# Kernel optimization log

Hardware: AMD Instinct MI355X
Metric: run time of the kernel (lower is better)

Reference implementation:

```python
import jax, jax.numpy as jnp
import numpy as np

HEADS = 48
HEAD_DIM = 64
DIM = 3072
RANK = 128
TEXT_LEN = 226
VID_LEN = 1822
B = 1
LORA_W = 1.0
EPS = 1e-5


def setup_inputs() -> dict:
    key = jax.random.key(0)
    ks = jax.random.split(key, 24)
    s = 0.02  # weight init scale
    inp = {
        "hidden_states": jax.random.normal(ks[0], (B, VID_LEN, DIM), jnp.float32),
        "encoder_hidden_states": jax.random.normal(ks[1], (B, TEXT_LEN, DIM), jnp.float32),
        "rope_cos": jax.random.uniform(ks[2], (VID_LEN, HEAD_DIM), jnp.float32),
        "rope_sin": jax.random.uniform(ks[3], (VID_LEN, HEAD_DIM), jnp.float32),
        "Wq": jax.random.normal(ks[4], (DIM, DIM), jnp.float32) * s,
        "bq": jax.random.normal(ks[5], (DIM,), jnp.float32) * s,
        "Wk": jax.random.normal(ks[6], (DIM, DIM), jnp.float32) * s,
        "bk": jax.random.normal(ks[7], (DIM,), jnp.float32) * s,
        "Wv": jax.random.normal(ks[8], (DIM, DIM), jnp.float32) * s,
        "bv": jax.random.normal(ks[9], (DIM,), jnp.float32) * s,
        "Wo": jax.random.normal(ks[10], (DIM, DIM), jnp.float32) * s,
        "bo": jax.random.normal(ks[11], (DIM,), jnp.float32) * s,
        "lq_down": jax.random.normal(ks[12], (RANK, DIM), jnp.float32) / RANK,
        "lq_up": jax.random.normal(ks[13], (DIM, RANK), jnp.float32) * s,
        "lk_down": jax.random.normal(ks[14], (RANK, DIM), jnp.float32) / RANK,
        "lk_up": jax.random.normal(ks[15], (DIM, RANK), jnp.float32) * s,
        "lv_down": jax.random.normal(ks[16], (RANK, DIM), jnp.float32) / RANK,
        "lv_up": jax.random.normal(ks[17], (DIM, RANK), jnp.float32) * s,
        "lp_down": jax.random.normal(ks[18], (RANK, DIM), jnp.float32) / RANK,
        "lp_up": jax.random.normal(ks[19], (DIM, RANK), jnp.float32) * s,
        "gamma_q": jnp.ones((HEAD_DIM,), jnp.float32),
        "beta_q": jnp.zeros((HEAD_DIM,), jnp.float32),
        "gamma_k": jnp.ones((HEAD_DIM,), jnp.float32),
        "beta_k": jnp.zeros((HEAD_DIM,), jnp.float32),
    }
    return inp


def _lora(x, down, up):
    # x: [B,S,DIM]; down: [RANK,DIM]; up: [DIM,RANK]
    return (x @ down.T) @ up.T


def _layernorm(x, gamma, beta):
    mu = jnp.mean(x, axis=-1, keepdims=True)
    var = jnp.mean(jnp.square(x - mu), axis=-1, keepdims=True)
    return (x - mu) * jax.lax.rsqrt(var + EPS) * gamma + beta


def _apply_rope(x, cos, sin):
    # diffusers apply_rotary_emb, use_real=True, unbind_dim=-1
    # x: [B,H,S,D]; cos/sin: [S,D]
    xr = x.reshape(*x.shape[:-1], HEAD_DIM // 2, 2)
    x1, x2 = xr[..., 0], xr[..., 1]
    x_rot = jnp.stack([-x2, x1], axis=-1).reshape(x.shape)
    return x * cos + x_rot * sin


def reference(hidden_states, encoder_hidden_states, rope_cos, rope_sin,
              Wq, bq, Wk, bk, Wv, bv, Wo, bo,
              lq_down, lq_up, lk_down, lk_up, lv_down, lv_up, lp_down, lp_up,
              gamma_q, beta_q, gamma_k, beta_k):
    h = jnp.concatenate([encoder_hidden_states, hidden_states], axis=1)  # [B,S,DIM]
    S = h.shape[1]

    q = h @ Wq.T + bq + _lora(h, lq_down, lq_up) * LORA_W
    k = h @ Wk.T + bk + _lora(h, lk_down, lk_up) * LORA_W
    v = h @ Wv.T + bv + _lora(h, lv_down, lv_up) * LORA_W

    def split_heads(x):  # [B,S,DIM] -> [B,H,S,D]
        return x.reshape(B, S, HEADS, HEAD_DIM).transpose(0, 2, 1, 3)

    q, k, v = split_heads(q), split_heads(k), split_heads(v)
    q = _layernorm(q, gamma_q, beta_q)
    k = _layernorm(k, gamma_k, beta_k)

    # RoPE on video tokens only
    q = q.at[:, :, TEXT_LEN:].set(_apply_rope(q[:, :, TEXT_LEN:], rope_cos, rope_sin))
    k = k.at[:, :, TEXT_LEN:].set(_apply_rope(k[:, :, TEXT_LEN:], rope_cos, rope_sin))

    # scaled dot-product attention (no mask, no dropout)
    scale = 1.0 / np.sqrt(HEAD_DIM).astype(np.float32)
    scores = jnp.einsum("bhqd,bhkd->bhqk", q, k) * scale
    probs = jax.nn.softmax(scores, axis=-1)
    attn_out = jnp.einsum("bhqk,bhkd->bhqd", probs, v)

    out = attn_out.transpose(0, 2, 1, 3).reshape(B, S, DIM)
    out = out @ Wo.T + bo + _lora(out, lp_down, lp_up) * LORA_W

    enc_out = out[:, :TEXT_LEN, :]
    hid_out = out[:, TEXT_LEN:, :]
    return (hid_out, enc_out)
```

## Files before the change

kernel.cpp:

```cpp
#include <hip/hip_runtime.h>
#include <hip/hip_bf16.h>
#include <stdint.h>

#define S_TOT 2048
#define TEXT 226
#define VID 1822
#define DIM 3072
#define NH 48
#define HD 64

typedef __bf16 bf16x8 __attribute__((ext_vector_type(8)));
typedef __bf16 bf16x4 __attribute__((ext_vector_type(4)));
typedef float f32x4 __attribute__((ext_vector_type(4)));

#define AS1 __attribute__((address_space(1)))
#define AS3 __attribute__((address_space(3)))

__device__ __forceinline__ void g2l16(const void* g, void* l) {
    __builtin_amdgcn_global_load_lds((const AS1 uint32_t*)(uintptr_t)g,
                                     (AS3 uint32_t*)(uintptr_t)l, 16, 0, 0);
}

__device__ __forceinline__ f32x4 mfma16(bf16x4 a, bf16x4 b, f32x4 c) {
#if __has_builtin(__builtin_amdgcn_mfma_f32_16x16x16bf16_1k)
    typedef short s4 __attribute__((ext_vector_type(4)));
    union U { bf16x4 b; s4 s; };
    U ua, ub; ua.b = a; ub.b = b;
    return __builtin_amdgcn_mfma_f32_16x16x16bf16_1k(ua.s, ub.s, c, 0, 0, 0);
#else
    f32x4 d = c;
    asm volatile("v_mfma_f32_16x16x16_bf16 %0, %1, %2, %0"
                 : "+v"(d) : "v"(a), "v"(b));
    return d;
#endif
}

#define ARENA_N 47431680ull

struct NormArgs { const void* p[24]; };

__global__ __launch_bounds__(256)
void normalize_inputs(NormArgs a, __bf16* __restrict__ arena)
{
    static constexpr unsigned long long segStart[25] = {
        0ull, 694272ull, 6291456ull, 15728640ull, 25165824ull, 34603008ull,
        44040192ull, 44433408ull, 44826624ull, 45219840ull, 45613056ull,
        46006272ull, 46399488ull, 46792704ull, 47185920ull, 47302528ull,
        47419136ull, 47422208ull, 47425280ull, 47428352ull, 47431424ull,
        47431488ull, 47431552ull, 47431616ull, 47431680ull };
    static constexpr int segIn[24] = {
        1, 0, 4, 6, 8, 10, 12, 13, 14, 15, 16, 17, 18, 19, 2, 3,
        5, 7, 9, 11, 20, 21, 22, 23 };

    const uint32_t w0 = *(const uint32_t*)a.p[20];
    const bool f32in = (w0 == 0x3F800000u);

    const size_t i0 = ((size_t)blockIdx.x * 256 + threadIdx.x) * 8;
    if (i0 >= ARENA_N) return;
    int s = 0;
    while (i0 >= segStart[s + 1]) s++;
    const size_t off = i0 - segStart[s];

    if (f32in) {
        const float* src = (const float*)a.p[segIn[s]] + off;
        const float4 v0 = ((const float4*)src)[0];
        const float4 v1 = ((const float4*)src)[1];
        bf16x8 o;
        o[0] = (__bf16)v0.x; o[1] = (__bf16)v0.y; o[2] = (__bf16)v0.z; o[3] = (__bf16)v0.w;
        o[4] = (__bf16)v1.x; o[5] = (__bf16)v1.y; o[6] = (__bf16)v1.z; o[7] = (__bf16)v1.w;
        *(bf16x8*)(arena + i0) = o;
    } else {
        const __bf16* src = (const __bf16*)a.p[segIn[s]] + off;
        *(uint4*)(arena + i0) = *(const uint4*)src;
    }
}

__device__ __forceinline__ void mm_chunks(
    const __bf16* __restrict__ Ag, int lda, const __bf16* __restrict__ Bg, int ldb,
    int kbeg, int kend, f32x4 (&acc)[4][4], __bf16* As, __bf16* Bs,
    int wave, int srow, int schk, int rdoff, int l15, int wm, int wn)
{
    for (int k0 = kbeg; k0 < kend; k0 += 32) {
        __syncthreads();
#pragma unroll
        for (int i = 0; i < 2; i++) {
            const int blk = i * 4 + wave;
            const int r = blk * 16 + srow;
            g2l16(Ag + (size_t)r * lda + k0 + schk, &As[blk * 512]);
            g2l16(Bg + (size_t)r * ldb + k0 + schk, &Bs[blk * 512]);
        }
        __syncthreads();
        bf16x8 af[4], bfr[4];
#pragma unroll
        for (int i = 0; i < 4; i++)
            af[i] = *(const bf16x8*)&As[(wm + i * 16 + l15) * 32 + rdoff];
#pragma unroll
        for (int j = 0; j < 4; j++)
            bfr[j] = *(const bf16x8*)&Bs[(wn + j * 16 + l15) * 32 + rdoff];
#pragma unroll
        for (int i = 0; i < 4; i++)
#pragma unroll
            for (int j = 0; j < 4; j++)
                acc[i][j] = __builtin_amdgcn_mfma_f32_16x16x32_bf16(af[i], bfr[j], acc[i][j], 0, 0, 0);
    }
}

template<int MODE>
__global__ __launch_bounds__(256)
void gemm_bt(const __bf16* __restrict__ A, int lda,
             const __bf16* __restrict__ B0, const __bf16* __restrict__ B1,
             const __bf16* __restrict__ B2, int ldb,
             const __bf16* __restrict__ bias0, const __bf16* __restrict__ bias1,
             const __bf16* __restrict__ bias2,
             __bf16* __restrict__ Cb, int ldc, int K, int tilesPerGroup,
             void* __restrict__ dout, const void* __restrict__ probe)
{
    __shared__ __bf16 As[128 * 32];
    __shared__ __bf16 Bs[128 * 32];
    const int tid  = threadIdx.x;
    const int wave = tid >> 6;
    const int lane = tid & 63;
    const int l15  = lane & 15, quad = lane >> 4;
    const int bm = blockIdx.x, bn = blockIdx.y;
    const int group = bn / tilesPerGroup;
    const int nt    = bn - group * tilesPerGroup;
    const __bf16* B    = (group == 0) ? B0 : ((group == 1) ? B1 : B2);
    const __bf16* bias = (group == 0) ? bias0 : ((group == 1) ? bias1 : bias2);

    const int srow  = lane >> 2;
    const int schk  = ((((lane & 3) - (lane >> 3)) & 3)) * 8;
    const int rdoff = ((quad + (l15 >> 1)) & 3) * 8;
    const __bf16* Ag = A + (size_t)(bm * 128) * lda;
    const __bf16* Bg = B + (size_t)(nt * 128) * ldb;

    f32x4 acc[4][4] = {};
    const int wm = (wave & 1) * 64;
    const int wn = (wave >> 1) * 64;

    mm_chunks(Ag, lda, Bg, ldb, 0, K, acc, As, Bs, wave, srow, schk, rdoff, l15, wm, wn);

    bool f32out = false;
    if (MODE == 1) f32out = (*(const uint32_t*)probe == 0x3F800000u);

#pragma unroll
    for (int i = 0; i < 4; i++) {
#pragma unroll
        for (int j = 0; j < 4; j++) {
            const int coll = wn + j * 16 + l15;
            const int col  = bn * 128 + coll;
            float bv = 0.f;
            if (bias) bv = (float)bias[nt * 128 + coll];
#pragma unroll
            for (int r = 0; r < 4; r++) {
                const int row = bm * 128 + wm + i * 16 + quad * 4 + r;
                float v = acc[i][j][r] + bv;
                if (MODE == 1) {
                    const size_t mrow = (row < TEXT) ? (size_t)(row + VID) : (size_t)(row - TEXT);
                    if (f32out) ((float*)dout)[mrow * DIM + col] = v;
                    else        ((__bf16*)dout)[mrow * DIM + col] = (__bf16)v;
                } else {
                    Cb[(size_t)row * ldc + col] = (__bf16)v;
                }
            }
        }
    }
}

#define QKV_NT 48
#define QKV_NI 24

__device__ __forceinline__ void barx() {
    asm volatile("" ::: "memory");
    __builtin_amdgcn_s_barrier();
    asm volatile("" ::: "memory");
}
__device__ __forceinline__ void vmw6() { asm volatile("s_waitcnt vmcnt(6)" ::: "memory"); }
__device__ __forceinline__ void vmw0() { asm volatile("s_waitcnt vmcnt(0)" ::: "memory"); }

__device__ __forceinline__ void stage2(const __bf16* gsrc, __bf16* lds, size_t koff) {
    g2l16(gsrc + koff,      lds);
    g2l16(gsrc + koff + 32, lds + 8192);
}

__global__ __launch_bounds__(512)
void gemm256_qkv(const __bf16* __restrict__ A,
                 const __bf16* __restrict__ B0, const __bf16* __restrict__ B1,
                 const __bf16* __restrict__ B2,
                 const __bf16* __restrict__ bias0, const __bf16* __restrict__ bias1,
                 const __bf16* __restrict__ bias2,
                 __bf16* __restrict__ C)
{
    __shared__ __bf16 L[65536];

    const int bid = blockIdx.x;
    const int swz = (bid & 7) * 32 + (bid >> 3);
    const int bm = swz & 7;
    const int bn = swz >> 3;
    const int group = bn / 12;
    const int nt    = bn - group * 12;
    const __bf16* Bm   = (group == 0) ? B0 : ((group == 1) ? B1 : B2);
    const __bf16* bias = (group == 0) ? bias0 : ((group == 1) ? bias1 : bias2);

    const int tid = threadIdx.x, wave = tid >> 6, lane = tid & 63;
    const int wr = wave >> 2, wc = wave & 3;
    const int l15 = lane & 15, quad = lane >> 4;
    const int srow  = lane >> 2;
    const int schk  = ((((lane & 3) - (lane >> 3)) & 3)) * 8;
    const int rdoff = ((quad + (l15 >> 1)) & 3) * 8;
    const int rdbase = l15 * 32 + rdoff;

    static constexpr int AL0[8] = {0,1,2,3, 8,9,10,11};
    static constexpr int AL1[8] = {4,5,6,7, 12,13,14,15};
    static constexpr int BL0[8] = {0,1,4,5, 8,9,12,13};
    static constexpr int BL1[8] = {2,3,6,7, 10,11,14,15};
    const int a0 = AL0[wave], a1 = AL1[wave], b0 = BL0[wave], b1 = BL1[wave];

    const __bf16* Ag = A  + (size_t)(bm * 256) * DIM;
    const __bf16* Bg = Bm + (size_t)(nt * 256) * DIM;
    const __bf16* gA0 = Ag + (size_t)(a0 * 16 + srow) * DIM + schk;
    const __bf16* gA1 = Ag + (size_t)(a1 * 16 + srow) * DIM + schk;
    const __bf16* gB0 = Bg + (size_t)(b0 * 16 + srow) * DIM + schk;
    const __bf16* gB1 = Bg + (size_t)(b1 * 16 + srow) * DIM + schk;

#define STG_A0(BUF, T) stage2(gA0, &L[(BUF)*32768 +         a0*512], (size_t)(T)*64)
#define STG_A1(BUF, T) stage2(gA1, &L[(BUF)*32768 +         a1*512], (size_t)(T)*64)
#define STG_B0(BUF, T) stage2(gB0, &L[(BUF)*32768 + 16384 + b0*512], (size_t)(T)*64)
#define STG_B1(BUF, T) stage2(gB1, &L[(BUF)*32768 + 16384 + b1*512], (size_t)(T)*64)

    f32x4 acc[8][4] = {};

    STG_A0(0, 0); STG_B0(0, 0); STG_A1(0, 0); STG_B1(0, 0);
    STG_A0(1, 1); STG_B0(1, 1); STG_A1(1, 1);
    vmw6();
    barx();

#define PH(BUF, MH, NH, STAGE, WAIT) do {                                        \
    bf16x8 af[4][2], bfr[2][2];                                                  \
    _Pragma("unroll")                                                            \
    for (int mm = 0; mm < 4; mm++) {                                             \
        af[mm][0] = *(const bf16x8*)&L[(BUF)*32768 +        (wr*8 + (MH)*4 + mm)*512 + rdbase]; \
        af[mm][1] = *(const bf16x8*)&L[(BUF)*32768 + 8192 + (wr*8 + (MH)*4 + mm)*512 + rdbase]; \
    }                                                                            \
    _Pragma("unroll")                                                            \
    for (int nn = 0; nn < 2; nn++) {                                             \
        bfr[nn][0] = *(const bf16x8*)&L[(BUF)*32768 + 16384 +        (wc*4 + (NH)*2 + nn)*512 + rdbase]; \
        bfr[nn][1] = *(const bf16x8*)&L[(BUF)*32768 + 16384 + 8192 + (wc*4 + (NH)*2 + nn)*512 + rdbase]; \
    }                                                                            \
    barx();                                                                      \
    STAGE;                                                                       \
    __builtin_amdgcn_s_setprio(1);                                               \
    _Pragma("unroll")                                                            \
    for (int mm = 0; mm < 4; mm++)                                               \
        _Pragma("unroll")                                                        \
        for (int nn = 0; nn < 2; nn++) {                                         \
            acc[(MH)*4+mm][(NH)*2+nn] = __builtin_amdgcn_mfma_f32_16x16x32_bf16( \
                af[mm][0], bfr[nn][0], acc[(MH)*4+mm][(NH)*2+nn], 0, 0, 0);      \
            acc[(MH)*4+mm][(NH)*2+nn] = __builtin_amdgcn_mfma_f32_16x16x32_bf16( \
                af[mm][1], bfr[nn][1], acc[(MH)*4+mm][(NH)*2+nn], 0, 0, 0);      \
        }                                                                        \
    __builtin_amdgcn_s_setprio(0);                                               \
    WAIT;                                                                        \
    barx();                                                                      \
} while (0)

#pragma unroll 1
    for (int i = 0; i < QKV_NI; i++) {
        const int t1 = 2 * i + 1, t2 = 2 * i + 2, t3 = 2 * i + 3;
        const bool more = (i < QKV_NI - 1);
        PH(0, 0, 0, { STG_B1(1, t1); },              { });
        PH(0, 0, 1, { if (more) STG_A0(0, t2); },    { });
        PH(0, 1, 0, { if (more) STG_B0(0, t2); },    { });
        PH(0, 1, 1, { if (more) STG_A1(0, t2); },    { if (more) vmw6(); else vmw0(); });
        PH(1, 0, 0, { if (more) STG_B1(0, t2); },    { });
        PH(1, 0, 1, { if (more) STG_A0(1, t3); },    { });
        PH(1, 1, 0, { if (more) STG_B0(1, t3); },    { });
        PH(1, 1, 1, { if (more) STG_A1(1, t3); },    { if (more) vmw6(); else vmw0(); });
    }
#undef PH
#undef STG_A0
#undef STG_A1
#undef STG_B0
#undef STG_B1

#pragma unroll
    for (int mh = 0; mh < 2; mh++)
#pragma unroll
    for (int nh = 0; nh < 2; nh++)
#pragma unroll
    for (int nn = 0; nn < 2; nn++) {
        const int coll = wc * 64 + nh * 32 + nn * 16 + l15;
        const float bv = (float)bias[nt * 256 + coll];
        const int col = bn * 256 + coll;
#pragma unroll
        for (int mm = 0; mm < 4; mm++) {
            const int rowb = bm * 256 + wr * 128 + mh * 64 + mm * 16 + quad * 4;
#pragma unroll
            for (int r = 0; r < 4; r++)
                C[(size_t)(rowb + r) * 9216 + col] = (__bf16)(acc[mh*4+mm][nh*2+nn][r] + bv);
        }
    }
}

struct TpArgs { const __bf16* S[4]; __bf16* D[4]; };

__global__ __launch_bounds__(256)
void transp_ld(TpArgs a)
{
    __shared__ float tile[64][65];
    const __bf16* src = a.S[blockIdx.z];
    __bf16* dst = a.D[blockIdx.z];
    const int j0 = blockIdx.x * 64;
    const int r0 = blockIdx.y * 64;
    const int tid = threadIdx.x;
    const int rr = tid >> 4;
    const int cc = (tid & 15) * 4;
#pragma unroll
    for (int p = 0; p < 4; p++) {
        const int r = p * 16 + rr;
        const uint2 raw = *(const uint2*)&src[(size_t)(r0 + r) * DIM + j0 + cc];
        const __bf16* b = (const __bf16*)&raw;
#pragma unroll
        for (int e = 0; e < 4; e++) tile[r][cc + e] = (float)b[e];
    }
    __syncthreads();
#pragma unroll
    for (int p = 0; p < 4; p++) {
        const int j = p * 16 + rr;
        __bf16 o[4];
#pragma unroll
        for (int e = 0; e < 4; e++) o[e] = (__bf16)tile[cc + e][j];
        *(uint2*)&dst[(size_t)(j0 + j) * 128 + r0 + cc] = *(const uint2*)o;
    }
}

struct FoldArgs { const __bf16* A[4]; const __bf16* B[4]; const __bf16* W[4]; __bf16* D[4]; };

__global__ __launch_bounds__(256)
void fold_w(FoldArgs a)
{
    __shared__ __bf16 As[128 * 32];
    __shared__ __bf16 Bs[128 * 32];
    const int z = blockIdx.z;
    const int tid  = threadIdx.x;
    const int wave = tid >> 6;
    const int lane = tid & 63;
    const int l15  = lane & 15, quad = lane >> 4;
    const int bm = blockIdx.x, bn = blockIdx.y;

    const int srow  = lane >> 2;
    const int schk  = ((((lane & 3) - (lane >> 3)) & 3)) * 8;
    const int rdoff = ((quad + (l15 >> 1)) & 3) * 8;
    const __bf16* Ag = a.A[z] + (size_t)(bm * 128) * 128;
    const __bf16* Bg = a.B[z] + (size_t)(bn * 128) * 128;
    const __bf16* W  = a.W[z];
    __bf16* D = a.D[z];

    f32x4 acc[4][4] = {};
    const int wm = (wave & 1) * 64;
    const int wn = (wave >> 1) * 64;

    mm_chunks(Ag, 128, Bg, 128, 0, 128, acc, As, Bs, wave, srow, schk, rdoff, l15, wm, wn);

#pragma unroll
    for (int i = 0; i < 4; i++) {
#pragma unroll
        for (int j = 0; j < 4; j++) {
            const int col = bn * 128 + wn + j * 16 + l15;
#pragma unroll
            for (int r = 0; r < 4; r++) {
                const int row = bm * 128 + wm + i * 16 + quad * 4 + r;
                const size_t idx = (size_t)row * DIM + col;
                D[idx] = (__bf16)(acc[i][j][r] + (float)W[idx]);
            }
        }
    }
}

__global__ __launch_bounds__(256)
void ln_vt(const __bf16* __restrict__ qkv,
           const __bf16* __restrict__ gq, const __bf16* __restrict__ bq,
           const __bf16* __restrict__ gk, const __bf16* __restrict__ bk,
           const __bf16* __restrict__ cosb, const __bf16* __restrict__ sinb,
           __bf16* __restrict__ qh, __bf16* __restrict__ kh,
           __bf16* __restrict__ vt)
{
    __shared__ float tile[64][65];
    if (blockIdx.x < 2048) {
        const int s = blockIdx.x;
        const int wave = threadIdx.x >> 6, lane = threadIdx.x & 63;
        for (int idx = wave; idx < 2 * NH; idx += 4) {
            const int mat  = idx / NH;
            const int head = idx - mat * NH;
            float x = (float)qkv[(size_t)s * 9216 + mat * DIM + head * HD + lane];
            float mu = x;
            mu += __shfl_xor(mu, 1, 64);  mu += __shfl_xor(mu, 2, 64);
            mu += __shfl_xor(mu, 4, 64);  mu += __shfl_xor(mu, 8, 64);
            mu += __shfl_xor(mu, 16, 64); mu += __shfl_xor(mu, 32, 64);
            mu *= 0.015625f;
            float d = x - mu;
            float vv = d * d;
            vv += __shfl_xor(vv, 1, 64);  vv += __shfl_xor(vv, 2, 64);
            vv += __shfl_xor(vv, 4, 64);  vv += __shfl_xor(vv, 8, 64);
            vv += __shfl_xor(vv, 16, 64); vv += __shfl_xor(vv, 32, 64);
            vv *= 0.015625f;
            const float g = (float)(mat ? gk[lane] : gq[lane]);
            const float b = (float)(mat ? bk[lane] : bq[lane]);
            float y = d * rsqrtf(vv + 1e-5f) * g + b;
            if (s >= TEXT) {
                const int pos = s - TEXT;
                const float c  = (float)cosb[pos * HD + lane];
                const float sn = (float)sinb[pos * HD + lane];
                const float oth = __shfl_xor(y, 1, 64);
                const float rot = (lane & 1) ? oth : -oth;
                y = y * c + rot * sn;
            }
            if (mat == 0) y *= 0.1803368801111137f;
            __bf16* dst = mat ? kh : qh;
            dst[((size_t)head * S_TOT + s) * HD + lane] = (__bf16)y;
        }
    } else {
        const int vb = blockIdx.x - 2048;
        const int h = vb >> 5, sb = vb & 31;
        const int tid = threadIdx.x;
        const int r0 = tid >> 4;
        const int c0 = (tid & 15) * 4;
#pragma unroll
        for (int p = 0; p < 4; p++) {
            const int r = p * 16 + r0;
            const uint2 raw = *(const uint2*)&qkv[((size_t)(sb * 64 + r)) * 9216 + 2 * DIM + h * HD + c0];
            const __bf16* b = (const __bf16*)&raw;
#pragma unroll
            for (int e = 0; e < 4; e++) tile[r][c0 + e] = (float)b[e];
        }
        __syncthreads();
#pragma unroll
        for (int p = 0; p < 4; p++) {
            const int d = p * 16 + r0;
            __bf16 o[4];
#pragma unroll
            for (int e = 0; e < 4; e++) o[e] = (__bf16)tile[c0 + e][d];
            *(uint2*)&vt[((size_t)(h * HD + d)) * S_TOT + sb * 64 + c0] = *(const uint2*)o;
        }
    }
}

#define KS_LD 72
#define VS_LD 146
#define NKB (S_TOT / 128)

__device__ __forceinline__ void fa_load(const __bf16* __restrict__ kh,
                                        const __bf16* __restrict__ vt,
                                        int h, int kb, int tid,
                                        bf16x8 (&kr)[4], bf16x8 (&vr)[4])
{
#pragma unroll
    for (int p = 0; p < 4; p++) {
        const int id = p * 256 + tid;
        const int krow = id >> 3, kc = (id & 7) * 8;
        kr[p] = *(const bf16x8*)(kh + ((size_t)(h * S_TOT + kb * 128 + krow)) * HD + kc);
        const int vrow = id >> 4, vc = (id & 15) * 8;
        vr[p] = *(const bf16x8*)(vt + ((size_t)(h * HD + vrow)) * S_TOT + kb * 128 + vc);
    }
}

__global__ __launch_bounds__(256)
void flash_attn(const __bf16* __restrict__ qh, const __bf16* __restrict__ kh,
                const __bf16* __restrict__ vt, __bf16* __restrict__ outp)
{
    __shared__ __bf16 Ks[128 * KS_LD];
    __shared__ __bf16 Vs[64 * VS_LD];
    const int qb = blockIdx.x, h = blockIdx.y;
    const int tid = threadIdx.x, wave = tid >> 6, lane = tid & 63;
    const int l15 = lane & 15, quad = lane >> 4;

    const __bf16* qp = qh + ((size_t)(h * S_TOT + qb * 64 + wave * 16 + l15)) * HD + quad * 8;
    const bf16x8 qf0 = *(const bf16x8*)qp;
    const bf16x8 qf1 = *(const bf16x8*)(qp + 32);

    f32x4 of[4] = {};
    float m_i = -1e30f, l_i = 0.f;

    bf16x8 kr[4], vr[4];
    fa_load(kh, vt, h, 0, tid, kr, vr);

    for (int kb = 0; kb < NKB; kb++) {
        __syncthreads();
#pragma unroll
        for (int p = 0; p < 4; p++) {
            const int id = p * 256 + tid;
            const int krow = id >> 3, kc = (id & 7) * 8;
            *(bf16x8*)&Ks[krow * KS_LD + kc] = kr[p];
            const int vrow = id >> 4, vc = (id & 15) * 8;
            *(bf16x8*)&Vs[vrow * VS_LD + vc] = vr[p];
        }
        __syncthreads();
        if (kb + 1 < NKB) fa_load(kh, vt, h, kb + 1, tid, kr, vr);

        f32x4 sf[8];
#pragma unroll
        for (int n = 0; n < 8; n++) {
            const bf16x8 k0 = *(const bf16x8*)&Ks[(n * 16 + l15) * KS_LD + quad * 8];
            const bf16x8 k1 = *(const bf16x8*)&Ks[(n * 16 + l15) * KS_LD + 32 + quad * 8];
            f32x4 z = {0.f, 0.f, 0.f, 0.f};
            z = __builtin_amdgcn_mfma_f32_16x16x32_bf16(k0, qf0, z, 0, 0, 0);
            sf[n] = __builtin_amdgcn_mfma_f32_16x16x32_bf16(k1, qf1, z, 0, 0, 0);
        }

        float mx = fmaxf(fmaxf(sf[0][0], sf[0][1]), fmaxf(sf[0][2], sf[0][3]));
#pragma unroll
        for (int n = 1; n < 8; n++)
            mx = fmaxf(mx, fmaxf(fmaxf(sf[n][0], sf[n][1]), fmaxf(sf[n][2], sf[n][3])));
        mx = fmaxf(mx, __shfl_xor(mx, 16, 64));
        mx = fmaxf(mx, __shfl_xor(mx, 32, 64));
        const float mnew = fmaxf(m_i, mx);
        const float alpha = __builtin_amdgcn_exp2f(m_i - mnew);
        m_i = mnew;
        float rs = 0.f;
#pragma unroll
        for (int n = 0; n < 8; n++)
#pragma unroll
            for (int r = 0; r < 4; r++) {
                const float pv = __builtin_amdgcn_exp2f(sf[n][r] - mnew);
                sf[n][r] = pv;
                rs += pv;
            }
        rs += __shfl_xor(rs, 16, 64);
        rs += __shfl_xor(rs, 32, 64);
        l_i = l_i * alpha + rs;

        bf16x4 pf[8];
#pragma unroll
        for (int kk = 0; kk < 8; kk++) {
            bf16x4 o;
            o[0] = (__bf16)sf[kk][0]; o[1] = (__bf16)sf[kk][1];
            o[2] = (__bf16)sf[kk][2]; o[3] = (__bf16)sf[kk][3];
            pf[kk] = o;
        }

#pragma unroll
        for (int r = 0; r < 4; r++) {
            const float a_r = __shfl(alpha, quad * 4 + r, 16);
#pragma unroll
            for (int j = 0; j < 4; j++) of[j][r] *= a_r;
        }

#pragma unroll
        for (int kk = 0; kk < 8; kk++) {
#pragma unroll
            for (int j = 0; j < 4; j++) {
                const bf16x4 vf = *(const bf16x4*)&Vs[(j * 16 + l15) * VS_LD + kk * 16 + quad * 4];
                of[j] = mfma16(pf[kk], vf, of[j]);
            }
        }
    }

#pragma unroll
    for (int r = 0; r < 4; r++) {
        const float lr = __shfl(l_i, quad * 4 + r, 16);
        const float inv = 1.f / lr;
        const int row = qb * 64 + wave * 16 + quad * 4 + r;
#pragma unroll
        for (int j = 0; j < 4; j++)
            outp[(size_t)row * DIM + h * HD + j * 16 + l15] = (__bf16)(of[j][r] * inv);
    }
}

extern "C" void kernel_launch(void* const* d_in, const int* in_sizes, int n_in,
                              void* d_out, int out_size, void* d_ws, size_t ws_size,
                              hipStream_t stream)
{
    char* ws = (char*)d_ws;
    __bf16* arena = (__bf16*)ws;

    const __bf16* h     = arena + 0;
    const __bf16* Wq    = arena + 6291456;
    const __bf16* Wk    = arena + 15728640;
    const __bf16* Wv    = arena + 25165824;
    const __bf16* Wo    = arena + 34603008;
    const __bf16* lqd   = arena + 44040192;
    const __bf16* lqu   = arena + 44433408;
    const __bf16* lkd   = arena + 44826624;
    const __bf16* lku   = arena + 45219840;
    const __bf16* lvd   = arena + 45613056;
    const __bf16* lvu   = arena + 46006272;
    const __bf16* lpd   = arena + 46399488;
    const __bf16* lpu   = arena + 46792704;
    const __bf16* ropec = arena + 47185920;
    const __bf16* ropes = arena + 47302528;
    const __bf16* bq    = arena + 47419136;
    const __bf16* bk    = arena + 47422208;
    const __bf16* bv    = arena + 47425280;
    const __bf16* bo    = arena + 47428352;
    const __bf16* gq    = arena + 47431424;
    const __bf16* btq   = arena + 47431488;
    const __bf16* gk    = arena + 47431552;
    const __bf16* btk   = arena + 47431616;

    __bf16* ldT  = (__bf16*)(ws + 94863360);
    __bf16* qkvb = (__bf16*)(ws + 98009088);
    __bf16* Wpo  = (__bf16*)(ws + 135757824);
    __bf16* Wpq  = (__bf16*)(ws + 154632192);
    __bf16* Wpk  = (__bf16*)(ws + 173506560);
    __bf16* Wpv  = (__bf16*)(ws + 192380928);
    __bf16* qh   = (__bf16*)(ws + 154632192);
    __bf16* kh   = (__bf16*)(ws + 179798016);
    __bf16* vt   = (__bf16*)(ws + 12582912);
    __bf16* attn = (__bf16*)(ws + 0);

    NormArgs na;
    for (int i = 0; i < 24; i++) na.p[i] = d_in[i];
    normalize_inputs<<<(unsigned)((ARENA_N / 8 + 255) / 256), 256, 0, stream>>>(na, arena);

    TpArgs tp;
    tp.S[0] = lqd; tp.S[1] = lkd; tp.S[2] = lvd; tp.S[3] = lpd;
    tp.D[0] = ldT; tp.D[1] = ldT + 393216; tp.D[2] = ldT + 786432; tp.D[3] = ldT + 1179648;
    transp_ld<<<dim3(48, 2, 4), 256, 0, stream>>>(tp);

    FoldArgs fa;
    fa.A[0] = lqu; fa.A[1] = lku; fa.A[2] = lvu; fa.A[3] = lpu;
    fa.B[0] = tp.D[0]; fa.B[1] = tp.D[1]; fa.B[2] = tp.D[2]; fa.B[3] = tp.D[3];
    fa.W[0] = Wq; fa.W[1] = Wk; fa.W[2] = Wv; fa.W[3] = Wo;
    fa.D[0] = Wpq; fa.D[1] = Wpk; fa.D[2] = Wpv; fa.D[3] = Wpo;
    fold_w<<<dim3(24, 24, 4), 256, 0, stream>>>(fa);

    gemm256_qkv<<<256, 512, 0, stream>>>(h, Wpq, Wpk, Wpv, bq, bk, bv, qkvb);
    gemm_bt<3><<<dim3(16, 8), 256, 0, stream>>>(
        h, DIM, Wpv + (size_t)2048 * DIM, Wpv + (size_t)2048 * DIM, Wpv + (size_t)2048 * DIM,
        DIM, bv + 2048, bv + 2048, bv + 2048,
        qkvb + 8192, 9216, DIM, 8, nullptr, nullptr);

    ln_vt<<<2048 + 1536, 256, 0, stream>>>(qkvb, gq, btq, gk, btk, ropec, ropes, qh, kh, vt);

    flash_attn<<<dim3(32, 48), 256, 0, stream>>>(qh, kh, vt, attn);

    gemm_bt<1><<<dim3(16, 24), 256, 0, stream>>>(
        attn, DIM, Wpo, Wpo, Wpo, DIM, bo, bo, bo,
        nullptr, DIM, DIM, 24, d_out, d_in[20]);
}
```

Baseline: 711.2 us.

## Shrink flash-attention KV tile to 64, raise occupancy, swizzle blocks per XCD

Halves the key/value tile per iteration from 128 to 64 rows, which cuts LDS and register use, and adds a launch-bounds occupancy hint of 6 blocks. The 2D grid becomes a 1D grid whose block index is remapped so that each XCD processes a contiguous group of heads, aiming for better L2 reuse of K/V. The trade-off is twice as many loop iterations and barriers, plus more frequent online-softmax rescaling.

```diff
diff --git a/kernel.cpp b/kernel.cpp
--- a/kernel.cpp
+++ b/kernel.cpp
@@ -444,32 +444,33 @@
     }
 }
 
-#define KS_LD 72
-#define VS_LD 146
-#define NKB (S_TOT / 128)
-
-__device__ __forceinline__ void fa_load(const __bf16* __restrict__ kh,
-                                        const __bf16* __restrict__ vt,
-                                        int h, int kb, int tid,
-                                        bf16x8 (&kr)[4], bf16x8 (&vr)[4])
-{
-#pragma unroll
-    for (int p = 0; p < 4; p++) {
+#define FA_LD 72
+#define NKB64 (S_TOT / 64)
+
+__device__ __forceinline__ void fa_load64(const __bf16* __restrict__ kh,
+                                          const __bf16* __restrict__ vt,
+                                          int h, int kb, int tid,
+                                          bf16x8 (&kr)[2], bf16x8 (&vr)[2])
+{
+#pragma unroll
+    for (int p = 0; p < 2; p++) {
         const int id = p * 256 + tid;
-        const int krow = id >> 3, kc = (id & 7) * 8;
-        kr[p] = *(const bf16x8*)(kh + ((size_t)(h * S_TOT + kb * 128 + krow)) * HD + kc);
-        const int vrow = id >> 4, vc = (id & 15) * 8;
-        vr[p] = *(const bf16x8*)(vt + ((size_t)(h * HD + vrow)) * S_TOT + kb * 128 + vc);
-    }
-}
-
-__global__ __launch_bounds__(256)
+        const int row = id >> 3;
+        const int c = (id & 7) * 8;
+        kr[p] = *(const bf16x8*)(kh + ((size_t)(h * S_TOT + kb * 64 + row)) * HD + c);
+        vr[p] = *(const bf16x8*)(vt + ((size_t)(h * HD + row)) * S_TOT + kb * 64 + c);
+    }
+}
+
+__global__ __launch_bounds__(256, 6)
 void flash_attn(const __bf16* __restrict__ qh, const __bf16* __restrict__ kh,
                 const __bf16* __restrict__ vt, __bf16* __restrict__ outp)
 {
-    __shared__ __bf16 Ks[128 * KS_LD];
-    __shared__ __bf16 Vs[64 * VS_LD];
-    const int qb = blockIdx.x, h = blockIdx.y;
+    __shared__ __bf16 Ks[64 * FA_LD];
+    __shared__ __bf16 Vs[64 * FA_LD];
+    const int swz = (blockIdx.x & 7) * 192 + (blockIdx.x >> 3);
+    const int h = swz >> 5;
+    const int qb = swz & 31;
     const int tid = threadIdx.x, wave = tid >> 6, lane = tid & 63;
     const int l15 = lane & 15, quad = lane >> 4;
 
@@ -480,27 +481,27 @@
     f32x4 of[4] = {};
     float m_i = -1e30f, l_i = 0.f;
 
-    bf16x8 kr[4], vr[4];
-    fa_load(kh, vt, h, 0, tid, kr, vr);
-
-    for (int kb = 0; kb < NKB; kb++) {
+    bf16x8 kr[2], vr[2];
+    fa_load64(kh, vt, h, 0, tid, kr, vr);
+
+    for (int kb = 0; kb < NKB64; kb++) {
         __syncthreads();
 #pragma unroll
-        for (int p = 0; p < 4; p++) {
+        for (int p = 0; p < 2; p++) {
             const int id = p * 256 + tid;
-            const int krow = id >> 3, kc = (id & 7) * 8;
-            *(bf16x8*)&Ks[krow * KS_LD + kc] = kr[p];
-            const int vrow = id >> 4, vc = (id & 15) * 8;
-            *(bf16x8*)&Vs[vrow * VS_LD + vc] = vr[p];
+            const int row = id >> 3;
+            const int c = (id & 7) * 8;
+            *(bf16x8*)&Ks[row * FA_LD + c] = kr[p];
+            *(bf16x8*)&Vs[row * FA_LD + c] = vr[p];
         }
         __syncthreads();
-        if (kb + 1 < NKB) fa_load(kh, vt, h, kb + 1, tid, kr, vr);
-
-        f32x4 sf[8];
-#pragma unroll
-        for (int n = 0; n < 8; n++) {
-            const bf16x8 k0 = *(const bf16x8*)&Ks[(n * 16 + l15) * KS_LD + quad * 8];
-            const bf16x8 k1 = *(const bf16x8*)&Ks[(n * 16 + l15) * KS_LD + 32 + quad * 8];
+        if (kb + 1 < NKB64) fa_load64(kh, vt, h, kb + 1, tid, kr, vr);
+
+        f32x4 sf[4];
+#pragma unroll
+        for (int n = 0; n < 4; n++) {
+            const bf16x8 k0 = *(const bf16x8*)&Ks[(n * 16 + l15) * FA_LD + quad * 8];
+            const bf16x8 k1 = *(const bf16x8*)&Ks[(n * 16 + l15) * FA_LD + 32 + quad * 8];
             f32x4 z = {0.f, 0.f, 0.f, 0.f};
             z = __builtin_amdgcn_mfma_f32_16x16x32_bf16(k0, qf0, z, 0, 0, 0);
             sf[n] = __builtin_amdgcn_mfma_f32_16x16x32_bf16(k1, qf1, z, 0, 0, 0);
@@ -508,7 +509,7 @@
 
         float mx = fmaxf(fmaxf(sf[0][0], sf[0][1]), fmaxf(sf[0][2], sf[0][3]));
 #pragma unroll
-        for (int n = 1; n < 8; n++)
+        for (int n = 1; n < 4; n++)
             mx = fmaxf(mx, fmaxf(fmaxf(sf[n][0], sf[n][1]), fmaxf(sf[n][2], sf[n][3])));
         mx = fmaxf(mx, __shfl_xor(mx, 16, 64));
         mx = fmaxf(mx, __shfl_xor(mx, 32, 64));
@@ -517,7 +518,7 @@
         m_i = mnew;
         float rs = 0.f;
 #pragma unroll
-        for (int n = 0; n < 8; n++)
+        for (int n = 0; n < 4; n++)
 #pragma unroll
             for (int r = 0; r < 4; r++) {
                 const float pv = __builtin_amdgcn_exp2f(sf[n][r] - mnew);
@@ -528,9 +529,9 @@
         rs += __shfl_xor(rs, 32, 64);
         l_i = l_i * alpha + rs;
 
-        bf16x4 pf[8];
-#pragma unroll
-        for (int kk = 0; kk < 8; kk++) {
+        bf16x4 pf[4];
+#pragma unroll
+        for (int kk = 0; kk < 4; kk++) {
             bf16x4 o;
             o[0] = (__bf16)sf[kk][0]; o[1] = (__bf16)sf[kk][1];
             o[2] = (__bf16)sf[kk][2]; o[3] = (__bf16)sf[kk][3];
@@ -545,10 +546,10 @@
         }
 
 #pragma unroll
-        for (int kk = 0; kk < 8; kk++) {
+        for (int kk = 0; kk < 4; kk++) {
 #pragma unroll
             for (int j = 0; j < 4; j++) {
-                const bf16x4 vf = *(const bf16x4*)&Vs[(j * 16 + l15) * VS_LD + kk * 16 + quad * 4];
+                const bf16x4 vf = *(const bf16x4*)&Vs[(j * 16 + l15) * FA_LD + kk * 16 + quad * 4];
                 of[j] = mfma16(pf[kk], vf, of[j]);
             }
         }
@@ -631,7 +632,7 @@
 
     ln_vt<<<2048 + 1536, 256, 0, stream>>>(qkvb, gq, btq, gk, btk, ropec, ropes, qh, kh, vt);
 
-    flash_attn<<<dim3(32, 48), 256, 0, stream>>>(qh, kh, vt, attn);
+    flash_attn<<<1536, 256, 0, stream>>>(qh, kh, vt, attn);
 
     gemm_bt<1><<<dim3(16, 24), 256, 0, stream>>>(
         attn, DIM, Wpo, Wpo, Wpo, DIM, bo, bo, bo,
```

Result: no change. 699.1 us (-1.7%).
